# Optimization experiments

Hardware: AMD Instinct MI355X
Metric: run time of the kernel (lower is better)

## Reference

```python
import jax, jax.numpy as jnp
import numpy as np

B, TQ, TV, D, U = 16, 64, 256, 512, 512

def setup_inputs() -> dict:
    key = jax.random.key(0)
    ks = jax.random.split(key, 9)
    s = 1.0 / np.sqrt(D)
    return {
        "query": jax.random.normal(ks[0], (B, TQ, D), dtype=jnp.float32),
        "values": jax.random.normal(ks[1], (B, TV, D), dtype=jnp.float32),
        "enc_mask": jax.random.randint(ks[2], (B, TV), 0, 2, dtype=jnp.int32),
        "W1": jax.random.normal(ks[3], (D, U), dtype=jnp.float32) * s,
        "b1": jnp.zeros((U,), dtype=jnp.float32),
        "W2": jax.random.normal(ks[4], (D, U), dtype=jnp.float32) * s,
        "b2": jnp.zeros((U,), dtype=jnp.float32),
        "Vw": jax.random.normal(ks[5], (U,), dtype=jnp.float32) * (1.0 / np.sqrt(U)),
        "Vb": jnp.zeros((), dtype=jnp.float32),
    }

def reference(query, values, enc_mask, W1, b1, W2, b2, Vw, Vb):
    # q_proj: [B,Tq,U]; v_proj: [B,Tv,U]
    q_proj = jnp.einsum("bqd,du->bqu", query, W1) + b1
    v_proj = jnp.einsum("bvd,du->bvu", values, W2) + b2
    # broadcast add -> [B,Tq,Tv,U], tanh, project to scalar score [B,Tq,Tv]
    s = jnp.tanh(q_proj[:, :, None, :] + v_proj[:, None, :, :])
    score = jnp.einsum("bqvu,u->bqv", s, Vw) + Vb
    # additive mask over encoder positions (mask[1] in the original call)
    score = score - (1.0 - enc_mask.astype(score.dtype))[:, None, :] * 1e9
    attn_weights = jax.nn.softmax(score, axis=2)  # [B,Tq,Tv]
    context = jnp.einsum("bqv,bvd->bqd", attn_weights, values)
    return (context, attn_weights)
```

## Files before the change

### kernel.cpp

```cpp
#include <hip/hip_runtime.h>

#define NB  16
#define NTQ 64
#define NTV 256
#define ND  512
#define NU  512

typedef _Float16 half8_t __attribute__((ext_vector_type(8)));
typedef _Float16 half4_t __attribute__((ext_vector_type(4)));
typedef _Float16 half2_t __attribute__((ext_vector_type(2)));
typedef float floatx4 __attribute__((ext_vector_type(4)));

#if __has_builtin(__builtin_amdgcn_fdot2)
#define FDOT2(a, b, c) __builtin_amdgcn_fdot2((a), (b), (c), false)
#else
#define FDOT2(a, b, c) ((c) + (float)((a)[0]) * (float)((b)[0]) + (float)((a)[1]) * (float)((b)[1]))
#endif
#if __has_builtin(__builtin_amdgcn_rcph)
#define RCPH(x) ((_Float16)__builtin_amdgcn_rcph((_Float16)(x)))
#else
#define RCPH(x) ((_Float16)__builtin_amdgcn_rcpf((float)(x)))
#endif

__device__ __forceinline__ float wred_sum(float x) {
#pragma unroll
    for (int m = 1; m < 64; m <<= 1) x += __shfl_xor(x, m, 64);
    return x;
}
__device__ __forceinline__ float wred_max(float x) {
#pragma unroll
    for (int m = 1; m < 64; m <<= 1) x = fmaxf(x, __shfl_xor(x, m, 64));
    return x;
}

__global__ __launch_bounds__(256) void prep_kernel(
        const float* __restrict__ W1, const float* __restrict__ W2,
        const float* __restrict__ Vw, const float* __restrict__ Vb,
        _Float16* __restrict__ W1T, _Float16* __restrict__ W2T,
        _Float16* __restrict__ Vwh, float* __restrict__ CVb) {
    const int blk = blockIdx.x;
    const int t = threadIdx.x;
    __shared__ float tb[32][33];
    if (blk < 512) {
        const float* W = (blk < 256) ? W1 : W2;
        _Float16* WT = (blk < 256) ? W1T : W2T;
        const int tile = blk & 255;
        const int tr = tile >> 4, tc = tile & 15;
        const int c = t & 31, r8 = t >> 5;
#pragma unroll
        for (int i = 0; i < 4; ++i) {
            int r = r8 + 8 * i;
            tb[r][c] = W[(tr * 32 + r) * 512 + tc * 32 + c];
        }
        __syncthreads();
#pragma unroll
        for (int i = 0; i < 4; ++i) {
            int r = r8 + 8 * i;
            WT[(tc * 32 + r) * 512 + tr * 32 + c] = (_Float16)tb[c][r];
        }
    } else {
        const float v0 = Vw[t], v1 = Vw[t + 256];
        Vwh[t] = (_Float16)v0;
        Vwh[t + 256] = (_Float16)v1;
        float s = wred_sum(v0 + v1);
        const int l = t & 63, w = t >> 6;
        __shared__ float ws4[4];
        if (l == 0) ws4[w] = s;
        __syncthreads();
        if (t == 0) CVb[0] = ws4[0] + ws4[1] + ws4[2] + ws4[3] + Vb[0];
    }
}

__global__ __launch_bounds__(256, 2) void proj_gemm_kernel(
        const float* __restrict__ query, const float* __restrict__ values,
        const _Float16* __restrict__ W1T, const _Float16* __restrict__ W2T,
        const float* __restrict__ b1, const float* __restrict__ b2,
        _Float16* __restrict__ Eqh, _Float16* __restrict__ Evp) {
    __shared__ __align__(16) _Float16 As[2][64 * 40];
    __shared__ __align__(16) _Float16 Bs[2][128 * 40];
    const float KC = 2.8853900817779268f;
    const int bid = blockIdx.x;
    const int t = threadIdx.x;
    const int l = t & 63, w = t >> 6;

    const float* Agf; const _Float16* Bg; const float* bias; _Float16* Cg;
    int mt, nt;
    if (bid < 64) {
        mt = bid >> 2; nt = bid & 3;
        Agf = query; Bg = W1T; bias = b1; Cg = Eqh;
    } else {
        const int vb = bid - 64;
        mt = vb >> 2; nt = vb & 3;
        Agf = values; Bg = W2T; bias = b2; Cg = Evp;
    }
    const int tm = mt * 64, tn = nt * 128;

    const int arow = t >> 2, acol = (t & 3) * 8;
    const int brow = t >> 1, bcol = (t & 1) * 16;
    const float* aptr = Agf + (tm + arow) * 512 + acol;
    const _Float16* bptr = Bg + (tn + brow) * 512 + bcol;

    const int wm = (w & 1) * 32, wn = (w >> 1) * 64;
    const int lr = l & 15, lk = l >> 4;

    floatx4 acc[2][4] = {};
    float4 ar0, ar1; half8_t br0, br1;

#define LOADK(kk) do { \
        const float* ap = aptr + (kk) * 32; \
        ar0 = *(const float4*)ap; ar1 = *(const float4*)(ap + 4); \
        const _Float16* bp = bptr + (kk) * 32; \
        br0 = *(const half8_t*)bp; br1 = *(const half8_t*)(bp + 8); \
    } while (0)
#define STOREK(buf) do { \
        half8_t h = {(_Float16)ar0.x, (_Float16)ar0.y, (_Float16)ar0.z, (_Float16)ar0.w, \
                     (_Float16)ar1.x, (_Float16)ar1.y, (_Float16)ar1.z, (_Float16)ar1.w}; \
        *(half8_t*)(As[buf] + arow * 40 + acol) = h; \
        *(half8_t*)(Bs[buf] + brow * 40 + bcol) = br0; \
        *(half8_t*)(Bs[buf] + brow * 40 + bcol + 8) = br1; \
    } while (0)

    LOADK(0);
    STOREK(0);
    __syncthreads();

    for (int kk = 0; kk < 16; ++kk) {
        const int cur = kk & 1;
        if (kk < 15) LOADK(kk + 1);
        half8_t af[2], bf[4];
#pragma unroll
        for (int i = 0; i < 2; ++i)
            af[i] = *(const half8_t*)(As[cur] + (wm + 16 * i + lr) * 40 + lk * 8);
#pragma unroll
        for (int j = 0; j < 4; ++j)
            bf[j] = *(const half8_t*)(Bs[cur] + (wn + 16 * j + lr) * 40 + lk * 8);
#pragma unroll
        for (int i = 0; i < 2; ++i)
#pragma unroll
            for (int j = 0; j < 4; ++j)
                acc[i][j] = __builtin_amdgcn_mfma_f32_16x16x32_f16(af[i], bf[j], acc[i][j], 0, 0, 0);
        if (kk < 15) STOREK(cur ^ 1);
        __syncthreads();
    }

#pragma unroll
    for (int i = 0; i < 2; ++i) {
#pragma unroll
        for (int j = 0; j < 4; ++j) {
            const int gr0 = tm + wm + 16 * i + lk * 4;
            const int gc = tn + wn + 16 * j + lr;
            const float bv = bias[gc];
#pragma unroll
            for (int r = 0; r < 4; ++r) {
                const float e = __builtin_amdgcn_exp2f(KC * (acc[i][j][r] + bv));
                Cg[(gr0 + r) * NU + gc] = (_Float16)fminf(e, 60000.f);
            }
        }
    }
#undef LOADK
#undef STOREK
}

__global__ __launch_bounds__(1024, 8) void score_kernel(
        const _Float16* __restrict__ Eqh, const _Float16* __restrict__ Evp,
        const _Float16* __restrict__ Vwh, const int* __restrict__ enc_mask,
        const float* __restrict__ CVbp, float* __restrict__ out) {
    const int bid = blockIdx.x;
    const int b = bid & 15, qp = bid >> 4;
    const int q0 = qp * 2;
    const int t = threadIdx.x;
    const int w = t >> 6, l = t & 63;
    const int qh = w & 1;
    const int vs = w >> 1;

    __shared__ float scL8[2][256][9];
    __shared__ float rs[2][4], ss[2][4];

    const half8_t eq8 = *(const half8_t*)(Eqh + (b * NTQ + q0 + qh) * NU + l * 8);
    const half8_t vw8 = *(const half8_t*)(Vwh + l * 8);
    const half2_t e0 = {eq8[0], eq8[1]}, e1 = {eq8[2], eq8[3]},
                  e2 = {eq8[4], eq8[5]}, e3 = {eq8[6], eq8[7]};
    const half2_t w0 = {vw8[0], vw8[1]}, w1 = {vw8[2], vw8[3]},
                  w2 = {vw8[4], vw8[5]}, w3 = {vw8[6], vw8[7]};
    const half2_t one2 = {(_Float16)1.0f, (_Float16)1.0f};

    int mv = 0;
    if (l < 32) mv = enc_mask[b * NTV + vs * 32 + l];
    const unsigned long long mbits = __ballot(mv != 0);

    const _Float16* evb = Evp + (b * NTV + vs * 32) * NU + l * 8;
#pragma unroll 4
    for (int r = 0; r < 32; ++r) {
        if ((mbits >> r) & 1ull) {
            const half8_t ev8 = *(const half8_t*)(evb + r * NU);
            const half2_t v0 = {ev8[0], ev8[1]}, v1 = {ev8[2], ev8[3]},
                          v2 = {ev8[4], ev8[5]}, v3 = {ev8[6], ev8[7]};
            const half2_t p0 = e0 * v0 + one2;
            const half2_t p1 = e1 * v1 + one2;
            const half2_t p2 = e2 * v2 + one2;
            const half2_t p3 = e3 * v3 + one2;
            const half2_t r0 = {RCPH(p0[0]), RCPH(p0[1])};
            const half2_t r1 = {RCPH(p1[0]), RCPH(p1[1])};
            const half2_t r2 = {RCPH(p2[0]), RCPH(p2[1])};
            const half2_t r3 = {RCPH(p3[0]), RCPH(p3[1])};
            float a0 = FDOT2(w0, r0, 0.f);
            a0 = FDOT2(w1, r1, a0);
            float a1 = FDOT2(w2, r2, 0.f);
            a1 = FDOT2(w3, r3, a1);
            float a = a0 + a1;
            a += __shfl_xor(a, 32, 64);
            a += __shfl_xor(a, 16, 64);
            a += __shfl_xor(a, 8, 64);
            if (l < 8) scL8[qh][vs * 32 + r][l] = a;
        } else {
            if (l < 8) scL8[qh][vs * 32 + r][l] = 0.f;
        }
    }
    __syncthreads();

    if (t < 512) {
        const int q = t >> 8, v = t & 255;
        const int ll = t & 63, w4 = (t >> 6) & 3;
        float s = 0.f;
#pragma unroll
        for (int i = 0; i < 8; ++i) s += scL8[q][v][i];
        float sc = CVbp[0] - 2.f * s;
        sc -= enc_mask[b * NTV + v] ? 0.f : 1e9f;
        float m = wred_max(sc);
        if (ll == 0) rs[q][w4] = m;
        __syncthreads();
        m = fmaxf(fmaxf(rs[q][0], rs[q][1]), fmaxf(rs[q][2], rs[q][3]));
        const float LOG2E = 1.4426950408889634f;
        const float ee = __builtin_amdgcn_exp2f((sc - m) * LOG2E);
        float t0 = wred_sum(ee);
        if (ll == 0) ss[q][w4] = t0;
        __syncthreads();
        const float S = (ss[q][0] + ss[q][1]) + (ss[q][2] + ss[q][3]);
        const float a = ee * __builtin_amdgcn_rcpf(S);
        float* out_attn = out + NB * NTQ * ND;
        out_attn[(b * NTQ + q0 + q) * NTV + v] = a;
    } else {
        __syncthreads();
        __syncthreads();
    }
}

__global__ __launch_bounds__(1024) void ctx_kernel(
        const float* __restrict__ values, float* __restrict__ out) {
    const int bid = blockIdx.x;
    const int b = bid & 15, qq = bid >> 4;
    const int q0 = qq * 4;
    const int t = threadIdx.x;

    __shared__ float attL[4][256];
    __shared__ float ctxp[4][4][516];

    const float* attn_in = out + NB * NTQ * ND;
    attL[t >> 8][t & 255] = attn_in[(b * NTQ + q0 + (t >> 8)) * NTV + (t & 255)];
    __syncthreads();

    {
        const int vg = t >> 8;
        const int dp = t & 255;
        const float* vsrc = values + (b * NTV + vg * 64) * ND + dp * 2;
        float c0x = 0.f, c0y = 0.f, c1x = 0.f, c1y = 0.f;
        float c2x = 0.f, c2y = 0.f, c3x = 0.f, c3y = 0.f;
#pragma unroll 4
        for (int vi = 0; vi < 64; ++vi) {
            const float2 vv = *(const float2*)(vsrc + vi * ND);
            const int v = vg * 64 + vi;
            const float aw0 = attL[0][v], aw1 = attL[1][v];
            const float aw2 = attL[2][v], aw3 = attL[3][v];
            c0x = fmaf(aw0, vv.x, c0x); c0y = fmaf(aw0, vv.y, c0y);
            c1x = fmaf(aw1, vv.x, c1x); c1y = fmaf(aw1, vv.y, c1y);
            c2x = fmaf(aw2, vv.x, c2x); c2y = fmaf(aw2, vv.y, c2y);
            c3x = fmaf(aw3, vv.x, c3x); c3y = fmaf(aw3, vv.y, c3y);
        }
        *(float2*)&ctxp[0][vg][dp * 2] = make_float2(c0x, c0y);
        *(float2*)&ctxp[1][vg][dp * 2] = make_float2(c1x, c1y);
        *(float2*)&ctxp[2][vg][dp * 2] = make_float2(c2x, c2y);
        *(float2*)&ctxp[3][vg][dp * 2] = make_float2(c3x, c3y);
    }
    __syncthreads();
#pragma unroll
    for (int k = 0; k < 2; ++k) {
        const int idx = t + k * 1024;
        const int cq = idx >> 9, d = idx & 511;
        float s = (ctxp[cq][0][d] + ctxp[cq][1][d]) + (ctxp[cq][2][d] + ctxp[cq][3][d]);
        out[(b * NTQ + q0 + cq) * ND + d] = s;
    }
}

extern "C" void kernel_launch(void* const* d_in, const int* in_sizes, int n_in,
                              void* d_out, int out_size, void* d_ws, size_t ws_size,
                              hipStream_t stream) {
    const float* query  = (const float*)d_in[0];
    const float* values = (const float*)d_in[1];
    const int*   emask  = (const int*)d_in[2];
    const float* W1     = (const float*)d_in[3];
    const float* b1     = (const float*)d_in[4];
    const float* W2     = (const float*)d_in[5];
    const float* b2     = (const float*)d_in[6];
    const float* Vw     = (const float*)d_in[7];
    const float* Vb     = (const float*)d_in[8];
    float* out = (float*)d_out;

    char* ws = (char*)d_ws;
    _Float16* W1T = (_Float16*)(ws + 0);
    _Float16* W2T = (_Float16*)(ws + 524288);
    _Float16* Eqh = (_Float16*)(ws + 6291456);
    _Float16* Evp = (_Float16*)(ws + 7340032);
    _Float16* Vwh = (_Float16*)(ws + 11534336);
    float* CVb    = (float*)(ws + 11539456);

    prep_kernel<<<dim3(513), dim3(256), 0, stream>>>(W1, W2, Vw, Vb, W1T, W2T, Vwh, CVb);
    proj_gemm_kernel<<<dim3(320), dim3(256), 0, stream>>>(query, values, W1T, W2T,
                                                          b1, b2, Eqh, Evp);
    score_kernel<<<dim3(512), dim3(1024), 0, stream>>>(Eqh, Evp, Vwh, emask, CVb, out);
    ctx_kernel<<<dim3(256), dim3(1024), 0, stream>>>(values, out);
}
```

Measured before the change: 52.40 us.

## Fuse score and context kernels, shrink GEMM M-tile, drop Vw prep

Merges the score/softmax kernel with the context kernel so attention weights stay in shared memory instead of being re-read from global memory, removing one launch. Each block now handles four queries with 64-row value slices. The projection GEMM tile is halved in M (640 blocks, higher occupancy bound) with an explicit X/Y register double-buffer. The Vw half conversion moves inline and the constant softmax bias is dropped, since softmax is shift-invariant. The fused kernel uses more shared memory and only 256 blocks, which lowers parallelism in the score phase.

```diff
diff --git a/kernel.cpp b/kernel.cpp
--- a/kernel.cpp
+++ b/kernel.cpp
@@ -35,48 +35,34 @@
 
 __global__ __launch_bounds__(256) void prep_kernel(
         const float* __restrict__ W1, const float* __restrict__ W2,
-        const float* __restrict__ Vw, const float* __restrict__ Vb,
-        _Float16* __restrict__ W1T, _Float16* __restrict__ W2T,
-        _Float16* __restrict__ Vwh, float* __restrict__ CVb) {
+        _Float16* __restrict__ W1T, _Float16* __restrict__ W2T) {
     const int blk = blockIdx.x;
     const int t = threadIdx.x;
     __shared__ float tb[32][33];
-    if (blk < 512) {
-        const float* W = (blk < 256) ? W1 : W2;
-        _Float16* WT = (blk < 256) ? W1T : W2T;
-        const int tile = blk & 255;
-        const int tr = tile >> 4, tc = tile & 15;
-        const int c = t & 31, r8 = t >> 5;
-#pragma unroll
-        for (int i = 0; i < 4; ++i) {
-            int r = r8 + 8 * i;
-            tb[r][c] = W[(tr * 32 + r) * 512 + tc * 32 + c];
-        }
-        __syncthreads();
-#pragma unroll
-        for (int i = 0; i < 4; ++i) {
-            int r = r8 + 8 * i;
-            WT[(tc * 32 + r) * 512 + tr * 32 + c] = (_Float16)tb[c][r];
-        }
-    } else {
-        const float v0 = Vw[t], v1 = Vw[t + 256];
-        Vwh[t] = (_Float16)v0;
-        Vwh[t + 256] = (_Float16)v1;
-        float s = wred_sum(v0 + v1);
-        const int l = t & 63, w = t >> 6;
-        __shared__ float ws4[4];
-        if (l == 0) ws4[w] = s;
-        __syncthreads();
-        if (t == 0) CVb[0] = ws4[0] + ws4[1] + ws4[2] + ws4[3] + Vb[0];
-    }
-}
-
-__global__ __launch_bounds__(256, 2) void proj_gemm_kernel(
+    const float* W = (blk < 256) ? W1 : W2;
+    _Float16* WT = (blk < 256) ? W1T : W2T;
+    const int tile = blk & 255;
+    const int tr = tile >> 4, tc = tile & 15;
+    const int c = t & 31, r8 = t >> 5;
+#pragma unroll
+    for (int i = 0; i < 4; ++i) {
+        int r = r8 + 8 * i;
+        tb[r][c] = W[(tr * 32 + r) * 512 + tc * 32 + c];
+    }
+    __syncthreads();
+#pragma unroll
+    for (int i = 0; i < 4; ++i) {
+        int r = r8 + 8 * i;
+        WT[(tc * 32 + r) * 512 + tr * 32 + c] = (_Float16)tb[c][r];
+    }
+}
+
+__global__ __launch_bounds__(256, 3) void proj_gemm_kernel(
         const float* __restrict__ query, const float* __restrict__ values,
         const _Float16* __restrict__ W1T, const _Float16* __restrict__ W2T,
         const float* __restrict__ b1, const float* __restrict__ b2,
         _Float16* __restrict__ Eqh, _Float16* __restrict__ Evp) {
-    __shared__ __align__(16) _Float16 As[2][64 * 40];
+    __shared__ __align__(16) _Float16 As[2][32 * 40];
     __shared__ __align__(16) _Float16 Bs[2][128 * 40];
     const float KC = 2.8853900817779268f;
     const int bid = blockIdx.x;
@@ -85,178 +71,175 @@
 
     const float* Agf; const _Float16* Bg; const float* bias; _Float16* Cg;
     int mt, nt;
-    if (bid < 64) {
+    if (bid < 128) {
         mt = bid >> 2; nt = bid & 3;
         Agf = query; Bg = W1T; bias = b1; Cg = Eqh;
     } else {
-        const int vb = bid - 64;
+        const int vb = bid - 128;
         mt = vb >> 2; nt = vb & 3;
         Agf = values; Bg = W2T; bias = b2; Cg = Evp;
     }
-    const int tm = mt * 64, tn = nt * 128;
-
-    const int arow = t >> 2, acol = (t & 3) * 8;
+    const int tm = mt * 32, tn = nt * 128;
+
+    const int arow = t >> 3, acol = (t & 7) * 4;
     const int brow = t >> 1, bcol = (t & 1) * 16;
     const float* aptr = Agf + (tm + arow) * 512 + acol;
     const _Float16* bptr = Bg + (tn + brow) * 512 + bcol;
 
-    const int wm = (w & 1) * 32, wn = (w >> 1) * 64;
+    const int wm = (w & 1) * 16, wn = (w >> 1) * 64;
     const int lr = l & 15, lk = l >> 4;
 
-    floatx4 acc[2][4] = {};
-    float4 ar0, ar1; half8_t br0, br1;
-
-#define LOADK(kk) do { \
-        const float* ap = aptr + (kk) * 32; \
-        ar0 = *(const float4*)ap; ar1 = *(const float4*)(ap + 4); \
-        const _Float16* bp = bptr + (kk) * 32; \
-        br0 = *(const half8_t*)bp; br1 = *(const half8_t*)(bp + 8); \
-    } while (0)
-#define STOREK(buf) do { \
-        half8_t h = {(_Float16)ar0.x, (_Float16)ar0.y, (_Float16)ar0.z, (_Float16)ar0.w, \
-                     (_Float16)ar1.x, (_Float16)ar1.y, (_Float16)ar1.z, (_Float16)ar1.w}; \
-        *(half8_t*)(As[buf] + arow * 40 + acol) = h; \
-        *(half8_t*)(Bs[buf] + brow * 40 + bcol) = br0; \
-        *(half8_t*)(Bs[buf] + brow * 40 + bcol + 8) = br1; \
-    } while (0)
-
-    LOADK(0);
-    STOREK(0);
-    __syncthreads();
-
-    for (int kk = 0; kk < 16; ++kk) {
-        const int cur = kk & 1;
-        if (kk < 15) LOADK(kk + 1);
-        half8_t af[2], bf[4];
-#pragma unroll
-        for (int i = 0; i < 2; ++i)
-            af[i] = *(const half8_t*)(As[cur] + (wm + 16 * i + lr) * 40 + lk * 8);
-#pragma unroll
-        for (int j = 0; j < 4; ++j)
-            bf[j] = *(const half8_t*)(Bs[cur] + (wn + 16 * j + lr) * 40 + lk * 8);
-#pragma unroll
-        for (int i = 0; i < 2; ++i)
-#pragma unroll
-            for (int j = 0; j < 4; ++j)
-                acc[i][j] = __builtin_amdgcn_mfma_f32_16x16x32_f16(af[i], bf[j], acc[i][j], 0, 0, 0);
-        if (kk < 15) STOREK(cur ^ 1);
+    floatx4 acc[4] = {};
+    float4 fX, fY; half8_t hX0, hX1, hY0, hY1;
+
+#define LOAD_X(kk) do { fX = *(const float4*)(aptr + (kk) * 32); \
+        hX0 = *(const half8_t*)(bptr + (kk) * 32); \
+        hX1 = *(const half8_t*)(bptr + (kk) * 32 + 8); } while (0)
+#define LOAD_Y(kk) do { fY = *(const float4*)(aptr + (kk) * 32); \
+        hY0 = *(const half8_t*)(bptr + (kk) * 32); \
+        hY1 = *(const half8_t*)(bptr + (kk) * 32 + 8); } while (0)
+#define STORE_X(buf) do { \
+        half4_t h = {(_Float16)fX.x, (_Float16)fX.y, (_Float16)fX.z, (_Float16)fX.w}; \
+        *(half4_t*)(As[buf] + arow * 40 + acol) = h; \
+        *(half8_t*)(Bs[buf] + brow * 40 + bcol) = hX0; \
+        *(half8_t*)(Bs[buf] + brow * 40 + bcol + 8) = hX1; } while (0)
+#define STORE_Y(buf) do { \
+        half4_t h = {(_Float16)fY.x, (_Float16)fY.y, (_Float16)fY.z, (_Float16)fY.w}; \
+        *(half4_t*)(As[buf] + arow * 40 + acol) = h; \
+        *(half8_t*)(Bs[buf] + brow * 40 + bcol) = hY0; \
+        *(half8_t*)(Bs[buf] + brow * 40 + bcol + 8) = hY1; } while (0)
+#define COMPUTE(buf) do { \
+        half8_t af = *(const half8_t*)(As[buf] + (wm + lr) * 40 + lk * 8); \
+        half8_t bf0 = *(const half8_t*)(Bs[buf] + (wn + lr) * 40 + lk * 8); \
+        half8_t bf1 = *(const half8_t*)(Bs[buf] + (wn + 16 + lr) * 40 + lk * 8); \
+        half8_t bf2 = *(const half8_t*)(Bs[buf] + (wn + 32 + lr) * 40 + lk * 8); \
+        half8_t bf3 = *(const half8_t*)(Bs[buf] + (wn + 48 + lr) * 40 + lk * 8); \
+        acc[0] = __builtin_amdgcn_mfma_f32_16x16x32_f16(af, bf0, acc[0], 0, 0, 0); \
+        acc[1] = __builtin_amdgcn_mfma_f32_16x16x32_f16(af, bf1, acc[1], 0, 0, 0); \
+        acc[2] = __builtin_amdgcn_mfma_f32_16x16x32_f16(af, bf2, acc[2], 0, 0, 0); \
+        acc[3] = __builtin_amdgcn_mfma_f32_16x16x32_f16(af, bf3, acc[3], 0, 0, 0); } while (0)
+
+    LOAD_X(0);
+    LOAD_Y(1);
+    STORE_X(0);
+    __syncthreads();
+
+#pragma unroll 1
+    for (int k2 = 0; k2 < 16; k2 += 2) {
+        if (k2 + 2 < 16) LOAD_X(k2 + 2);
+        COMPUTE(0);
+        STORE_Y(1);
         __syncthreads();
-    }
-
-#pragma unroll
-    for (int i = 0; i < 2; ++i) {
-#pragma unroll
-        for (int j = 0; j < 4; ++j) {
-            const int gr0 = tm + wm + 16 * i + lk * 4;
-            const int gc = tn + wn + 16 * j + lr;
-            const float bv = bias[gc];
-#pragma unroll
-            for (int r = 0; r < 4; ++r) {
-                const float e = __builtin_amdgcn_exp2f(KC * (acc[i][j][r] + bv));
-                Cg[(gr0 + r) * NU + gc] = (_Float16)fminf(e, 60000.f);
+        if (k2 + 3 < 16) LOAD_Y(k2 + 3);
+        COMPUTE(1);
+        if (k2 + 2 < 16) STORE_X(0);
+        __syncthreads();
+    }
+
+#pragma unroll
+    for (int j = 0; j < 4; ++j) {
+        const int gr0 = tm + wm + lk * 4;
+        const int gc = tn + wn + 16 * j + lr;
+        const float bv = bias[gc];
+#pragma unroll
+        for (int r = 0; r < 4; ++r) {
+            const float e = __builtin_amdgcn_exp2f(KC * (acc[j][r] + bv));
+            Cg[(gr0 + r) * NU + gc] = (_Float16)fminf(e, 60000.f);
+        }
+    }
+#undef LOAD_X
+#undef LOAD_Y
+#undef STORE_X
+#undef STORE_Y
+#undef COMPUTE
+}
+
+__global__ __launch_bounds__(1024) void score_ctx_kernel(
+        const _Float16* __restrict__ Eqh, const _Float16* __restrict__ Evp,
+        const float* __restrict__ Vw, const int* __restrict__ enc_mask,
+        const float* __restrict__ values, float* __restrict__ out) {
+    const int bid = blockIdx.x;
+    const int b = bid & 15, qq = bid >> 4;
+    const int q0 = qq * 4;
+    const int t = threadIdx.x;
+    const int w = t >> 6, l = t & 63;
+    const int qh = w & 3;
+    const int vs = w >> 2;
+
+    __shared__ float scL8[4][256][9];
+    __shared__ float attL[4][256];
+    __shared__ float ctxp[4][4][516];
+    __shared__ float rs[4][4], ss[4][4];
+
+    {
+        const half8_t eq8 = *(const half8_t*)(Eqh + (b * NTQ + q0 + qh) * NU + l * 8);
+        const float4 vwf0 = *(const float4*)(Vw + l * 8);
+        const float4 vwf1 = *(const float4*)(Vw + l * 8 + 4);
+        const half2_t e0 = {eq8[0], eq8[1]}, e1 = {eq8[2], eq8[3]},
+                      e2 = {eq8[4], eq8[5]}, e3 = {eq8[6], eq8[7]};
+        const half2_t w0 = {(_Float16)vwf0.x, (_Float16)vwf0.y},
+                      w1 = {(_Float16)vwf0.z, (_Float16)vwf0.w},
+                      w2 = {(_Float16)vwf1.x, (_Float16)vwf1.y},
+                      w3 = {(_Float16)vwf1.z, (_Float16)vwf1.w};
+        const half2_t one2 = {(_Float16)1.0f, (_Float16)1.0f};
+
+        const int mv = enc_mask[b * NTV + vs * 64 + l];
+        const unsigned long long mbits = __ballot(mv != 0);
+
+        const _Float16* evb = Evp + (b * NTV + vs * 64) * NU + l * 8;
+#pragma unroll 4
+        for (int r = 0; r < 64; ++r) {
+            if ((mbits >> r) & 1ull) {
+                const half8_t ev8 = *(const half8_t*)(evb + r * NU);
+                const half2_t v0 = {ev8[0], ev8[1]}, v1 = {ev8[2], ev8[3]},
+                              v2 = {ev8[4], ev8[5]}, v3 = {ev8[6], ev8[7]};
+                const half2_t p0 = e0 * v0 + one2;
+                const half2_t p1 = e1 * v1 + one2;
+                const half2_t p2 = e2 * v2 + one2;
+                const half2_t p3 = e3 * v3 + one2;
+                const half2_t r0 = {RCPH(p0[0]), RCPH(p0[1])};
+                const half2_t r1 = {RCPH(p1[0]), RCPH(p1[1])};
+                const half2_t r2 = {RCPH(p2[0]), RCPH(p2[1])};
+                const half2_t r3 = {RCPH(p3[0]), RCPH(p3[1])};
+                float a0 = FDOT2(w0, r0, 0.f);
+                a0 = FDOT2(w1, r1, a0);
+                float a1 = FDOT2(w2, r2, 0.f);
+                a1 = FDOT2(w3, r3, a1);
+                float a = a0 + a1;
+                a += __shfl_xor(a, 32, 64);
+                a += __shfl_xor(a, 16, 64);
+                a += __shfl_xor(a, 8, 64);
+                if (l < 8) scL8[qh][vs * 64 + r][l] = a;
+            } else {
+                if (l < 8) scL8[qh][vs * 64 + r][l] = 0.f;
             }
         }
     }
-#undef LOADK
-#undef STOREK
-}
-
-__global__ __launch_bounds__(1024, 8) void score_kernel(
-        const _Float16* __restrict__ Eqh, const _Float16* __restrict__ Evp,
-        const _Float16* __restrict__ Vwh, const int* __restrict__ enc_mask,
-        const float* __restrict__ CVbp, float* __restrict__ out) {
-    const int bid = blockIdx.x;
-    const int b = bid & 15, qp = bid >> 4;
-    const int q0 = qp * 2;
-    const int t = threadIdx.x;
-    const int w = t >> 6, l = t & 63;
-    const int qh = w & 1;
-    const int vs = w >> 1;
-
-    __shared__ float scL8[2][256][9];
-    __shared__ float rs[2][4], ss[2][4];
-
-    const half8_t eq8 = *(const half8_t*)(Eqh + (b * NTQ + q0 + qh) * NU + l * 8);
-    const half8_t vw8 = *(const half8_t*)(Vwh + l * 8);
-    const half2_t e0 = {eq8[0], eq8[1]}, e1 = {eq8[2], eq8[3]},
-                  e2 = {eq8[4], eq8[5]}, e3 = {eq8[6], eq8[7]};
-    const half2_t w0 = {vw8[0], vw8[1]}, w1 = {vw8[2], vw8[3]},
-                  w2 = {vw8[4], vw8[5]}, w3 = {vw8[6], vw8[7]};
-    const half2_t one2 = {(_Float16)1.0f, (_Float16)1.0f};
-
-    int mv = 0;
-    if (l < 32) mv = enc_mask[b * NTV + vs * 32 + l];
-    const unsigned long long mbits = __ballot(mv != 0);
-
-    const _Float16* evb = Evp + (b * NTV + vs * 32) * NU + l * 8;
-#pragma unroll 4
-    for (int r = 0; r < 32; ++r) {
-        if ((mbits >> r) & 1ull) {
-            const half8_t ev8 = *(const half8_t*)(evb + r * NU);
-            const half2_t v0 = {ev8[0], ev8[1]}, v1 = {ev8[2], ev8[3]},
-                          v2 = {ev8[4], ev8[5]}, v3 = {ev8[6], ev8[7]};
-            const half2_t p0 = e0 * v0 + one2;
-            const half2_t p1 = e1 * v1 + one2;
-            const half2_t p2 = e2 * v2 + one2;
-            const half2_t p3 = e3 * v3 + one2;
-            const half2_t r0 = {RCPH(p0[0]), RCPH(p0[1])};
-            const half2_t r1 = {RCPH(p1[0]), RCPH(p1[1])};
-            const half2_t r2 = {RCPH(p2[0]), RCPH(p2[1])};
-            const half2_t r3 = {RCPH(p3[0]), RCPH(p3[1])};
-            float a0 = FDOT2(w0, r0, 0.f);
-            a0 = FDOT2(w1, r1, a0);
-            float a1 = FDOT2(w2, r2, 0.f);
-            a1 = FDOT2(w3, r3, a1);
-            float a = a0 + a1;
-            a += __shfl_xor(a, 32, 64);
-            a += __shfl_xor(a, 16, 64);
-            a += __shfl_xor(a, 8, 64);
-            if (l < 8) scL8[qh][vs * 32 + r][l] = a;
-        } else {
-            if (l < 8) scL8[qh][vs * 32 + r][l] = 0.f;
-        }
-    }
-    __syncthreads();
-
-    if (t < 512) {
-        const int q = t >> 8, v = t & 255;
-        const int ll = t & 63, w4 = (t >> 6) & 3;
+    __syncthreads();
+
+    const int q = t >> 8, v = t & 255;
+    const int w4 = (t >> 6) & 3;
+    {
         float s = 0.f;
 #pragma unroll
         for (int i = 0; i < 8; ++i) s += scL8[q][v][i];
-        float sc = CVbp[0] - 2.f * s;
+        float sc = -2.f * s;
         sc -= enc_mask[b * NTV + v] ? 0.f : 1e9f;
         float m = wred_max(sc);
-        if (ll == 0) rs[q][w4] = m;
+        if (l == 0) rs[q][w4] = m;
         __syncthreads();
         m = fmaxf(fmaxf(rs[q][0], rs[q][1]), fmaxf(rs[q][2], rs[q][3]));
         const float LOG2E = 1.4426950408889634f;
         const float ee = __builtin_amdgcn_exp2f((sc - m) * LOG2E);
         float t0 = wred_sum(ee);
-        if (ll == 0) ss[q][w4] = t0;
+        if (l == 0) ss[q][w4] = t0;
         __syncthreads();
         const float S = (ss[q][0] + ss[q][1]) + (ss[q][2] + ss[q][3]);
         const float a = ee * __builtin_amdgcn_rcpf(S);
+        attL[q][v] = a;
         float* out_attn = out + NB * NTQ * ND;
         out_attn[(b * NTQ + q0 + q) * NTV + v] = a;
-    } else {
-        __syncthreads();
-        __syncthreads();
-    }
-}
-
-__global__ __launch_bounds__(1024) void ctx_kernel(
-        const float* __restrict__ values, float* __restrict__ out) {
-    const int bid = blockIdx.x;
-    const int b = bid & 15, qq = bid >> 4;
-    const int q0 = qq * 4;
-    const int t = threadIdx.x;
-
-    __shared__ float attL[4][256];
-    __shared__ float ctxp[4][4][516];
-
-    const float* attn_in = out + NB * NTQ * ND;
-    attL[t >> 8][t & 255] = attn_in[(b * NTQ + q0 + (t >> 8)) * NTV + (t & 255)];
+    }
     __syncthreads();
 
     {
@@ -268,9 +251,9 @@
 #pragma unroll 4
         for (int vi = 0; vi < 64; ++vi) {
             const float2 vv = *(const float2*)(vsrc + vi * ND);
-            const int v = vg * 64 + vi;
-            const float aw0 = attL[0][v], aw1 = attL[1][v];
-            const float aw2 = attL[2][v], aw3 = attL[3][v];
+            const int vv_i = vg * 64 + vi;
+            const float aw0 = attL[0][vv_i], aw1 = attL[1][vv_i];
+            const float aw2 = attL[2][vv_i], aw3 = attL[3][vv_i];
             c0x = fmaf(aw0, vv.x, c0x); c0y = fmaf(aw0, vv.y, c0y);
             c1x = fmaf(aw1, vv.x, c1x); c1y = fmaf(aw1, vv.y, c1y);
             c2x = fmaf(aw2, vv.x, c2x); c2y = fmaf(aw2, vv.y, c2y);
@@ -302,7 +285,6 @@
     const float* W2     = (const float*)d_in[5];
     const float* b2     = (const float*)d_in[6];
     const float* Vw     = (const float*)d_in[7];
-    const float* Vb     = (const float*)d_in[8];
     float* out = (float*)d_out;
 
     char* ws = (char*)d_ws;
@@ -310,12 +292,9 @@
     _Float16* W2T = (_Float16*)(ws + 524288);
     _Float16* Eqh = (_Float16*)(ws + 6291456);
     _Float16* Evp = (_Float16*)(ws + 7340032);
-    _Float16* Vwh = (_Float16*)(ws + 11534336);
-    float* CVb    = (float*)(ws + 11539456);
-
-    prep_kernel<<<dim3(513), dim3(256), 0, stream>>>(W1, W2, Vw, Vb, W1T, W2T, Vwh, CVb);
-    proj_gemm_kernel<<<dim3(320), dim3(256), 0, stream>>>(query, values, W1T, W2T,
+
+    prep_kernel<<<dim3(512), dim3(256), 0, stream>>>(W1, W2, W1T, W2T);
+    proj_gemm_kernel<<<dim3(640), dim3(256), 0, stream>>>(query, values, W1T, W2T,
                                                           b1, b2, Eqh, Evp);
-    score_kernel<<<dim3(512), dim3(1024), 0, stream>>>(Eqh, Evp, Vwh, emask, CVb, out);
-    ctx_kernel<<<dim3(256), dim3(1024), 0, stream>>>(values, out);
-}
+    score_ctx_kernel<<<dim3(256), dim3(1024), 0, stream>>>(Eqh, Evp, Vw, emask, values, out);
+}
```

Measured after the change: 54.14 us. 3.3% more time.
